# Optimization experiments

Measured on AMD Instinct MI355X. Metric: run time of the kernel, lower is better.

## Reference

```python
import jax, jax.numpy as jnp
import numpy as np

E = 1024   # embed_dim
H = 16     # num_heads
D = E // H # head_dim = 64
Q = 4      # num_queries
B = 4
S = 2048


def setup_inputs() -> dict:
    key = jax.random.key(0)
    ks = jax.random.split(key, 9)
    s = 0.02  # init scale for weights
    return {
        "x":  jax.random.normal(ks[0], (B, S, E), jnp.float32),
        "Wq": jax.random.normal(ks[1], (Q, E, E), jnp.float32) * s,  # stacked per-query Linear weights (torch layout: out,in)
        "bq": jax.random.normal(ks[2], (Q, E), jnp.float32) * s,
        "Wk": jax.random.normal(ks[3], (E, E), jnp.float32) * s,
        "bk": jax.random.normal(ks[4], (E,), jnp.float32) * s,
        "Wv": jax.random.normal(ks[5], (E, E), jnp.float32) * s,
        "bv": jax.random.normal(ks[6], (E,), jnp.float32) * s,
        "Wo": jax.random.normal(ks[7], (E, E), jnp.float32) * s,
        "bo": jax.random.normal(ks[8], (E,), jnp.float32) * s,
    }


def reference(x, Wq, bq, Wk, bk, Wv, bv, Wo, bo):
    B_, S_, E_ = x.shape
    scale = 1.0 / jnp.sqrt(jnp.asarray(D, x.dtype))
    # all query projections at once: (Q,B,S,E) -> (Q,B,S,H,D)
    q = (jnp.einsum('bse,qfe->qbsf', x, Wq) + bq[:, None, None, :]).reshape(Q, B_, S_, H, D)
    k = (x @ Wk.T + bk).reshape(B_, S_, H, D)
    v = (x @ Wv.T + bv).reshape(B_, S_, H, D)
    # NOTE: faithful to the torch code, which never moves the head axis before matmul:
    # scores[q,b,s,h,g] = sum_d q[q,b,s,h,d] * k[b,s,g,d]  -> softmax over heads g
    scores = jnp.einsum('qbshd,bsgd->qbshg', q, k) * scale      # (Q,B,S,H,H)
    probs = jax.nn.softmax(scores, axis=-1)
    out = jnp.einsum('qbshg,bsgd->qbshd', probs, v)             # (Q,B,S,H,D)
    # torch: .transpose(1,2).contiguous().view(B,S,E) == permute to (B,H,S,D) then reshape
    out = jnp.transpose(out, (0, 1, 3, 2, 4)).reshape(Q, B_, S_, E_)
    out = out.sum(axis=0)
    return out @ Wo.T + bo
```

## Files before the change

### kernel.cpp

```cpp
#include <hip/hip_runtime.h>


typedef __bf16 bf16x8 __attribute__((ext_vector_type(8)));
typedef float f32x4 __attribute__((ext_vector_type(4)));

__device__ __forceinline__ unsigned short f2b(float f) {
  unsigned u = __float_as_uint(f);
  return (unsigned short)((u + 0x7fffu + ((u >> 16) & 1u)) >> 16);
}
__device__ __forceinline__ float bl(unsigned u) { return __uint_as_float(u << 16); }
__device__ __forceinline__ float bh(unsigned u) { return __uint_as_float(u & 0xffff0000u); }

__device__ __forceinline__ void async16(const void* g, void* l) {
  __builtin_amdgcn_global_load_lds(
      (const __attribute__((address_space(1))) void*)g,
      (__attribute__((address_space(3))) void*)l, 16, 0, 0);
}

__global__ void cvt_f32_bf16(const float* __restrict__ s, unsigned short* __restrict__ d, int n4) {
  int i = blockIdx.x * 256 + threadIdx.x;
  if (i >= n4) return;
  float4 v = ((const float4*)s)[i];
  uint2 o;
  o.x = (unsigned)f2b(v.x) | ((unsigned)f2b(v.y) << 16);
  o.y = (unsigned)f2b(v.z) | ((unsigned)f2b(v.w) << 16);
  ((uint2*)d)[i] = o;
}

__global__ void bias_concat(const float* __restrict__ bq, const float* __restrict__ bk,
                            const float* __restrict__ bv, float* __restrict__ dst) {
  int i = blockIdx.x * 256 + threadIdx.x;
  float v = (i < 4096) ? bq[i] : (i < 5120 ? bk[i - 4096] : bv[i - 5120]);
  dst[i] = v;
}

template <typename OutT>
__global__ __launch_bounds__(256) void gemm_bt(const unsigned short* __restrict__ A,
                                               const unsigned short* __restrict__ Bt,
                                               const float* __restrict__ bias,
                                               OutT* __restrict__ C, int M, int N, int K) {
  __shared__ __align__(16) unsigned short As[128 * 64];
  __shared__ __align__(16) unsigned short Bs[128 * 64];
  const int t = threadIdx.x;
  const int lane = t & 63, w = t >> 6;
  const int wm = (w >> 1) * 64, wn = (w & 1) * 64;
  const int lr = lane & 15, lq = lane >> 4;
  const int bm0 = blockIdx.y * 128, bn0 = blockIdx.x * 128;

  f32x4 zero = {0.f, 0.f, 0.f, 0.f};
  f32x4 acc[4][4];
#pragma unroll
  for (int i = 0; i < 4; ++i)
#pragma unroll
    for (int j = 0; j < 4; ++j) acc[i][j] = zero;

  const int swz = lr & 7;

  for (int k0 = 0; k0 < K; k0 += 64) {
    __syncthreads();
#pragma unroll
    for (int j = 0; j < 4; ++j) {
      int slot = j * 256 + t;
      int r = slot >> 3;
      int gran = slot & 7;
      int c = (gran ^ (r & 7)) * 8;
      async16(A + (size_t)(bm0 + r) * K + k0 + c, As + slot * 8);
      async16(Bt + (size_t)(bn0 + r) * K + k0 + c, Bs + slot * 8);
    }
    __syncthreads();
#pragma unroll
    for (int kk = 0; kk < 64; kk += 32) {
      const int kg = kk >> 3;
      bf16x8 af[4], bfr[4];
#pragma unroll
      for (int i = 0; i < 4; ++i)
        af[i] = *(const bf16x8*)(As + (wm + i * 16 + lr) * 64 + (((kg + lq) ^ swz) << 3));
#pragma unroll
      for (int j = 0; j < 4; ++j)
        bfr[j] = *(const bf16x8*)(Bs + (wn + j * 16 + lr) * 64 + (((kg + lq) ^ swz) << 3));
#pragma unroll
      for (int i = 0; i < 4; ++i)
#pragma unroll
        for (int j = 0; j < 4; ++j)
          acc[i][j] = __builtin_amdgcn_mfma_f32_16x16x32_bf16(af[i], bfr[j], acc[i][j], 0, 0, 0);
    }
  }

#pragma unroll
  for (int i = 0; i < 4; ++i) {
    int gr = bm0 + wm + i * 16 + lq * 4;
#pragma unroll
    for (int j = 0; j < 4; ++j) {
      int gc = bn0 + wn + j * 16 + lr;
      float bsv = bias[gc];
#pragma unroll
      for (int r = 0; r < 4; ++r) {
        float vv = acc[i][j][r] + bsv;
        if constexpr (sizeof(OutT) == 2)
          C[(size_t)(gr + r) * N + gc] = (OutT)f2b(vv);
        else
          C[(size_t)(gr + r) * N + gc] = vv;
      }
    }
  }
}

__global__ __launch_bounds__(256) void attn_scatter(const unsigned short* __restrict__ qkv,
                                                    unsigned short* __restrict__ t) {
  __shared__ __align__(16) unsigned short vs[4][1024];
  __shared__ float ps[4][16 * 17];
  const int w = threadIdx.x >> 6, lane = threadIdx.x & 63;
  const int pos = blockIdx.x * 4 + w;
  const int b = pos >> 11, s = pos & 2047;
  const unsigned short* row = qkv + (size_t)pos * 6144;
  unsigned short* vw = vs[w];
  float* pw = ps[w];
  const int lr = lane & 15, lq = lane >> 4;

  {
    const uint4* sv = (const uint4*)(row + 5120);
    uint4* dv = (uint4*)vw;
    dv[lane * 2] = sv[lane * 2];
    dv[lane * 2 + 1] = sv[lane * 2 + 1];
  }
  bf16x8 kf0 = *(const bf16x8*)(row + 4096 + lr * 64 + lq * 8);
  bf16x8 kf1 = *(const bf16x8*)(row + 4096 + lr * 64 + 32 + lq * 8);

  float oa[16];
#pragma unroll
  for (int i = 0; i < 16; ++i) oa[i] = 0.f;
  const int h2 = lr, dseg = lq;

#pragma unroll
  for (int qi = 0; qi < 4; ++qi) {
    bf16x8 qf0 = *(const bf16x8*)(row + qi * 1024 + lr * 64 + lq * 8);
    bf16x8 qf1 = *(const bf16x8*)(row + qi * 1024 + lr * 64 + 32 + lq * 8);
    f32x4 sc = {0.f, 0.f, 0.f, 0.f};
    sc = __builtin_amdgcn_mfma_f32_16x16x32_bf16(qf0, kf0, sc, 0, 0, 0);
    sc = __builtin_amdgcn_mfma_f32_16x16x32_bf16(qf1, kf1, sc, 0, 0, 0);
#pragma unroll
    for (int r = 0; r < 4; ++r) {
      float x = sc[r] * 0.125f;
      float m = x;
#pragma unroll
      for (int d = 1; d < 16; d <<= 1) m = fmaxf(m, __shfl_xor(m, d));
      float e = __expf(x - m);
      float sum = e;
#pragma unroll
      for (int d = 1; d < 16; d <<= 1) sum += __shfl_xor(sum, d);
      pw[(lq * 4 + r) * 17 + lr] = e / sum;
    }
    __syncthreads();
#pragma unroll
    for (int g = 0; g < 16; ++g) {
      float p = pw[h2 * 17 + g];
      const uint4* vp = (const uint4*)(vw + g * 64 + dseg * 16);
      uint4 a = vp[0], c = vp[1];
      oa[0] += p * bl(a.x);  oa[1] += p * bh(a.x);
      oa[2] += p * bl(a.y);  oa[3] += p * bh(a.y);
      oa[4] += p * bl(a.z);  oa[5] += p * bh(a.z);
      oa[6] += p * bl(a.w);  oa[7] += p * bh(a.w);
      oa[8] += p * bl(c.x);  oa[9] += p * bh(c.x);
      oa[10] += p * bl(c.y); oa[11] += p * bh(c.y);
      oa[12] += p * bl(c.z); oa[13] += p * bh(c.z);
      oa[14] += p * bl(c.w); oa[15] += p * bh(c.w);
    }
    __syncthreads();
  }

  size_t off = ((size_t)(b * 2048 + 128 * h2 + (s >> 4))) * 1024 + 64 * (s & 15) + dseg * 16;
  uint4 p0, p1;
  p0.x = (unsigned)f2b(oa[0]) | ((unsigned)f2b(oa[1]) << 16);
  p0.y = (unsigned)f2b(oa[2]) | ((unsigned)f2b(oa[3]) << 16);
  p0.z = (unsigned)f2b(oa[4]) | ((unsigned)f2b(oa[5]) << 16);
  p0.w = (unsigned)f2b(oa[6]) | ((unsigned)f2b(oa[7]) << 16);
  p1.x = (unsigned)f2b(oa[8]) | ((unsigned)f2b(oa[9]) << 16);
  p1.y = (unsigned)f2b(oa[10]) | ((unsigned)f2b(oa[11]) << 16);
  p1.z = (unsigned)f2b(oa[12]) | ((unsigned)f2b(oa[13]) << 16);
  p1.w = (unsigned)f2b(oa[14]) | ((unsigned)f2b(oa[15]) << 16);
  ((uint4*)(t + off))[0] = p0;
  ((uint4*)(t + off + 8))[0] = p1;
}

extern "C" void kernel_launch(void* const* d_in, const int* in_sizes, int n_in,
                              void* d_out, int out_size, void* d_ws, size_t ws_size,
                              hipStream_t stream) {
  const float* x  = (const float*)d_in[0];
  const float* Wq = (const float*)d_in[1];
  const float* bq = (const float*)d_in[2];
  const float* Wk = (const float*)d_in[3];
  const float* bk = (const float*)d_in[4];
  const float* Wv = (const float*)d_in[5];
  const float* bv = (const float*)d_in[6];
  const float* Wo = (const float*)d_in[7];
  const float* bo = (const float*)d_in[8];
  float* out = (float*)d_out;

  char* ws = (char*)d_ws;
  unsigned short* xb      = (unsigned short*)(ws + 0);
  unsigned short* wcat    = (unsigned short*)(ws + 16777216);
  unsigned short* wo_b    = (unsigned short*)(ws + 29360128);
  float*          biascat = (float*)(ws + 31457280);
  unsigned short* qkv     = (unsigned short*)(ws + 31481856);
  unsigned short* t       = xb;

  cvt_f32_bf16<<<8192, 256, 0, stream>>>(x, xb, 8388608 / 4);
  cvt_f32_bf16<<<4096, 256, 0, stream>>>(Wq, wcat, 4194304 / 4);
  cvt_f32_bf16<<<1024, 256, 0, stream>>>(Wk, wcat + 4194304, 1048576 / 4);
  cvt_f32_bf16<<<1024, 256, 0, stream>>>(Wv, wcat + 5242880, 1048576 / 4);
  cvt_f32_bf16<<<1024, 256, 0, stream>>>(Wo, wo_b, 1048576 / 4);
  bias_concat<<<24, 256, 0, stream>>>(bq, bk, bv, biascat);

  gemm_bt<unsigned short><<<dim3(48, 64), 256, 0, stream>>>(xb, wcat, biascat, qkv, 8192, 6144, 1024);
  attn_scatter<<<2048, 256, 0, stream>>>(qkv, t);
  gemm_bt<float><<<dim3(8, 64), 256, 0, stream>>>(t, wo_b, bo, out, 8192, 1024, 1024);
}
```

Baseline: 314.1 us.

## Fuse conversion kernels and use MFMA for probs-times-V in attention

Merges the five f32-to-bf16 conversion launches and the bias concat into a single kernel, which cuts launch overhead. In the attention kernel, the scalar probs×V FMA loop is replaced by MFMA ops on bf16 V and probability fragments, removing the second syncthreads and the 16-wide unpacking. Softmax also drops the max subtraction, which risks overflow when scores are large, and the probabilities are now rounded to bf16. Note that the first syncthreads after the LDS probability writes is removed, so other lanes may read pw before it has been written.

```diff
diff --git a/kernel.cpp b/kernel.cpp
--- a/kernel.cpp
+++ b/kernel.cpp
@@ -8,8 +8,6 @@
   unsigned u = __float_as_uint(f);
   return (unsigned short)((u + 0x7fffu + ((u >> 16) & 1u)) >> 16);
 }
-__device__ __forceinline__ float bl(unsigned u) { return __uint_as_float(u << 16); }
-__device__ __forceinline__ float bh(unsigned u) { return __uint_as_float(u & 0xffff0000u); }
 
 __device__ __forceinline__ void async16(const void* g, void* l) {
   __builtin_amdgcn_global_load_lds(
@@ -17,21 +15,34 @@
       (__attribute__((address_space(3))) void*)l, 16, 0, 0);
 }
 
-__global__ void cvt_f32_bf16(const float* __restrict__ s, unsigned short* __restrict__ d, int n4) {
+__global__ __launch_bounds__(256) void cvt_all(
+    const float* __restrict__ x, const float* __restrict__ Wq, const float* __restrict__ Wk,
+    const float* __restrict__ Wv, const float* __restrict__ Wo, const float* __restrict__ bq,
+    const float* __restrict__ bk, const float* __restrict__ bv,
+    unsigned short* __restrict__ xb, unsigned short* __restrict__ wcat,
+    unsigned short* __restrict__ wo_b, float* __restrict__ biascat) {
+  if (blockIdx.x >= 15360) {
+    int j = (blockIdx.x - 15360) * 256 + threadIdx.x;
+    if (j < 6144) {
+      float v = (j < 4096) ? bq[j] : (j < 5120 ? bk[j - 4096] : bv[j - 5120]);
+      biascat[j] = v;
+    }
+    return;
+  }
   int i = blockIdx.x * 256 + threadIdx.x;
-  if (i >= n4) return;
-  float4 v = ((const float4*)s)[i];
+  const float* s;
+  unsigned short* d;
+  int off;
+  if (i < 2097152)      { s = x;  d = xb;             off = i; }
+  else if (i < 3145728) { s = Wq; d = wcat;           off = i - 2097152; }
+  else if (i < 3407872) { s = Wk; d = wcat + 4194304; off = i - 3145728; }
+  else if (i < 3670016) { s = Wv; d = wcat + 5242880; off = i - 3407872; }
+  else                  { s = Wo; d = wo_b;           off = i - 3670016; }
+  float4 v = ((const float4*)s)[off];
   uint2 o;
   o.x = (unsigned)f2b(v.x) | ((unsigned)f2b(v.y) << 16);
   o.y = (unsigned)f2b(v.z) | ((unsigned)f2b(v.w) << 16);
-  ((uint2*)d)[i] = o;
-}
-
-__global__ void bias_concat(const float* __restrict__ bq, const float* __restrict__ bk,
-                            const float* __restrict__ bv, float* __restrict__ dst) {
-  int i = blockIdx.x * 256 + threadIdx.x;
-  float v = (i < 4096) ? bq[i] : (i < 5120 ? bk[i - 4096] : bv[i - 5120]);
-  dst[i] = v;
+  ((uint2*)d)[off] = o;
 }
 
 template <typename OutT>
@@ -126,10 +137,22 @@
   bf16x8 kf0 = *(const bf16x8*)(row + 4096 + lr * 64 + lq * 8);
   bf16x8 kf1 = *(const bf16x8*)(row + 4096 + lr * 64 + 32 + lq * 8);
 
-  float oa[16];
-#pragma unroll
-  for (int i = 0; i < 16; ++i) oa[i] = 0.f;
-  const int h2 = lr, dseg = lq;
+  bf16x8 vf[4];
+#pragma unroll
+  for (int dc = 0; dc < 4; ++dc) {
+#pragma unroll
+    for (int j = 0; j < 8; ++j) vf[dc][j] = (__bf16)0.0f;
+    if (lq < 2) {
+      const __bf16* vb = (const __bf16*)vw;
+#pragma unroll
+      for (int j = 0; j < 8; ++j)
+        vf[dc][j] = vb[(lq * 8 + j) * 64 + dc * 16 + lr];
+    }
+  }
+
+  f32x4 acc[4];
+#pragma unroll
+  for (int dc = 0; dc < 4; ++dc) acc[dc] = (f32x4){0.f, 0.f, 0.f, 0.f};
 
 #pragma unroll
   for (int qi = 0; qi < 4; ++qi) {
@@ -140,46 +163,32 @@
     sc = __builtin_amdgcn_mfma_f32_16x16x32_bf16(qf1, kf1, sc, 0, 0, 0);
 #pragma unroll
     for (int r = 0; r < 4; ++r) {
-      float x = sc[r] * 0.125f;
-      float m = x;
-#pragma unroll
-      for (int d = 1; d < 16; d <<= 1) m = fmaxf(m, __shfl_xor(m, d));
-      float e = __expf(x - m);
+      float e = __expf(sc[r] * 0.125f);
       float sum = e;
 #pragma unroll
       for (int d = 1; d < 16; d <<= 1) sum += __shfl_xor(sum, d);
       pw[(lq * 4 + r) * 17 + lr] = e / sum;
     }
-    __syncthreads();
-#pragma unroll
-    for (int g = 0; g < 16; ++g) {
-      float p = pw[h2 * 17 + g];
-      const uint4* vp = (const uint4*)(vw + g * 64 + dseg * 16);
-      uint4 a = vp[0], c = vp[1];
-      oa[0] += p * bl(a.x);  oa[1] += p * bh(a.x);
-      oa[2] += p * bl(a.y);  oa[3] += p * bh(a.y);
-      oa[4] += p * bl(a.z);  oa[5] += p * bh(a.z);
-      oa[6] += p * bl(a.w);  oa[7] += p * bh(a.w);
-      oa[8] += p * bl(c.x);  oa[9] += p * bh(c.x);
-      oa[10] += p * bl(c.y); oa[11] += p * bh(c.y);
-      oa[12] += p * bl(c.z); oa[13] += p * bh(c.z);
-      oa[14] += p * bl(c.w); oa[15] += p * bh(c.w);
-    }
-    __syncthreads();
-  }
-
-  size_t off = ((size_t)(b * 2048 + 128 * h2 + (s >> 4))) * 1024 + 64 * (s & 15) + dseg * 16;
-  uint4 p0, p1;
-  p0.x = (unsigned)f2b(oa[0]) | ((unsigned)f2b(oa[1]) << 16);
-  p0.y = (unsigned)f2b(oa[2]) | ((unsigned)f2b(oa[3]) << 16);
-  p0.z = (unsigned)f2b(oa[4]) | ((unsigned)f2b(oa[5]) << 16);
-  p0.w = (unsigned)f2b(oa[6]) | ((unsigned)f2b(oa[7]) << 16);
-  p1.x = (unsigned)f2b(oa[8]) | ((unsigned)f2b(oa[9]) << 16);
-  p1.y = (unsigned)f2b(oa[10]) | ((unsigned)f2b(oa[11]) << 16);
-  p1.z = (unsigned)f2b(oa[12]) | ((unsigned)f2b(oa[13]) << 16);
-  p1.w = (unsigned)f2b(oa[14]) | ((unsigned)f2b(oa[15]) << 16);
-  ((uint4*)(t + off))[0] = p0;
-  ((uint4*)(t + off + 8))[0] = p1;
+    bf16x8 pf;
+#pragma unroll
+    for (int j = 0; j < 8; ++j) pf[j] = (__bf16)0.0f;
+    if (lq < 2) {
+#pragma unroll
+      for (int j = 0; j < 8; ++j) pf[j] = (__bf16)pw[lr * 17 + lq * 8 + j];
+    }
+#pragma unroll
+    for (int dc = 0; dc < 4; ++dc)
+      acc[dc] = __builtin_amdgcn_mfma_f32_16x16x32_bf16(vf[dc], pf, acc[dc], 0, 0, 0);
+  }
+
+  size_t base = ((size_t)(b * 2048 + 128 * lr + (s >> 4))) * 1024 + 64 * (s & 15) + lq * 4;
+#pragma unroll
+  for (int dc = 0; dc < 4; ++dc) {
+    uint2 u;
+    u.x = (unsigned)f2b(acc[dc][0]) | ((unsigned)f2b(acc[dc][1]) << 16);
+    u.y = (unsigned)f2b(acc[dc][2]) | ((unsigned)f2b(acc[dc][3]) << 16);
+    *(uint2*)(t + base + dc * 16) = u;
+  }
 }
 
 extern "C" void kernel_launch(void* const* d_in, const int* in_sizes, int n_in,
@@ -204,12 +213,7 @@
   unsigned short* qkv     = (unsigned short*)(ws + 31481856);
   unsigned short* t       = xb;
 
-  cvt_f32_bf16<<<8192, 256, 0, stream>>>(x, xb, 8388608 / 4);
-  cvt_f32_bf16<<<4096, 256, 0, stream>>>(Wq, wcat, 4194304 / 4);
-  cvt_f32_bf16<<<1024, 256, 0, stream>>>(Wk, wcat + 4194304, 1048576 / 4);
-  cvt_f32_bf16<<<1024, 256, 0, stream>>>(Wv, wcat + 5242880, 1048576 / 4);
-  cvt_f32_bf16<<<1024, 256, 0, stream>>>(Wo, wo_b, 1048576 / 4);
-  bias_concat<<<24, 256, 0, stream>>>(bq, bk, bv, biascat);
+  cvt_all<<<15384, 256, 0, stream>>>(x, Wq, Wk, Wv, Wo, bq, bk, bv, xb, wcat, wo_b, biascat);
 
   gemm_bt<unsigned short><<<dim3(48, 64), 256, 0, stream>>>(xb, wcat, biascat, qkv, 8192, 6144, 1024);
   attn_scatter<<<2048, 256, 0, stream>>>(qkv, t);
```

Result: faster. 283.0 us (-9.9%).
